# Kernel tuning notes

Measured on AMD Instinct MI355X. Metric: run time of the kernel, lower is better.

The kernel has to match this reference:

```python
import jax, jax.numpy as jnp
import numpy as np
import math

B, S, H = 8, 1024, 1024
LN_EPS = 1e-5  # assumed epsilon of create_normalization_layer('layer_norm')


def setup_inputs() -> dict:
    key = jax.random.key(0)
    ks = jax.random.split(key, 6)
    context = jax.random.normal(ks[0], (B, S, H), dtype=jnp.float32)
    mask = jnp.ones((B, 1, S), dtype=jnp.int32)
    prior = jax.random.uniform(ks[1], (B, S, S), dtype=jnp.float32)
    # LayerNorm params
    gamma = jnp.ones((H,), dtype=jnp.float32)
    beta = jnp.zeros((H,), dtype=jnp.float32)
    # Dense projections (Glorot-like init)
    scale = 1.0 / np.sqrt(H)
    Wk = jax.random.normal(ks[2], (H, H), dtype=jnp.float32) * scale
    bk = jnp.zeros((H,), dtype=jnp.float32)
    Wq = jax.random.normal(ks[3], (H, H), dtype=jnp.float32) * scale
    bq = jnp.zeros((H,), dtype=jnp.float32)
    return {"context": context, "mask": mask, "prior": prior,
            "gamma": gamma, "beta": beta, "Wk": Wk, "bk": bk, "Wq": Wq, "bq": bq}


def reference(context, mask, prior, gamma, beta, Wk, bk, Wq, bq):
    dtype = context.dtype
    s = context.shape[1]
    hs = context.shape[2]
    i = jnp.arange(s)
    adj_upper = i[:, None] == (i[None, :] - 1)          # [S,S] superdiagonal
    adj_lower = i[:, None] == (i[None, :] + 1)          # subdiagonal
    adj_mask = adj_upper | adj_lower
    pad = mask[:, 0, :].astype(bool)                    # [B,S]
    pad2d = pad[:, :, None] & pad[:, None, :]           # [B,S,S]
    final_adj = adj_mask[None, :, :] & pad2d

    # LayerNorm over last axis
    mu = jnp.mean(context, axis=-1, keepdims=True)
    var = jnp.mean(jnp.square(context - mu), axis=-1, keepdims=True)
    cn = (context - mu) * jax.lax.rsqrt(var + LN_EPS) * gamma + beta

    k = cn @ Wk + bk                                    # [B,S,H]
    q = cn @ Wq + bq
    scores = jnp.einsum('bsh,bth->bst', q, k) / math.sqrt(hs)
    scores = jnp.where(final_adj, scores, jnp.asarray(-1e9, dtype))
    neibor = jax.nn.softmax(scores, axis=-1)
    neibor = jnp.sqrt(neibor * jnp.swapaxes(neibor, 1, 2) + 1e-9)
    neibor = prior + (1.0 - prior) * neibor

    triu = i[None, :] >= i[:, None]                     # [S,S] upper incl diag
    tri = triu.astype(dtype)
    b_eye = jnp.eye(s, dtype=bool)

    t = jnp.log(neibor + 1e-9)
    t = jnp.where(adj_upper[None, :, :], t, jnp.asarray(0.0, dtype))
    t = jnp.einsum('bij,jk->bik', t, tri)               # cumulative over cols
    g = jnp.exp(jnp.einsum('ij,bjk->bik', tri, t))      # hierarchical prefix product
    keep = jnp.logical_not(jnp.logical_xor(triu, b_eye))
    g = jnp.where(keep[None, :, :], g, jnp.asarray(0.0, dtype))
    neibor_diag = jnp.where(b_eye[None, :, :], jnp.asarray(1e-9, dtype), neibor)
    g = g + jnp.swapaxes(g, 1, 2) + neibor_diag
    g = g / (jnp.sum(g, axis=-1, keepdims=True) + 1e-9)

    f2d = pad2d.astype(dtype)
    g = g * f2d
    neibor = neibor * f2d
    return g, neibor
```

## Files before the change

### kernel.cpp

```cpp
#include <hip/hip_runtime.h>
#include <hip/hip_bf16.h>

#define SB 8
#define SS 1024
#define SH 1024
#define LN_EPS 1e-5f

typedef unsigned short u16;
typedef __attribute__((ext_vector_type(8))) short bf16x8;
typedef __attribute__((ext_vector_type(4))) float f32x4;

__device__ __forceinline__ u16 f2bf(float f) {
  __hip_bfloat16 h = __float2bfloat16(f);
  return *reinterpret_cast<u16*>(&h);
}

__device__ __forceinline__ void gld16(const void* g, void* l) {
  __builtin_amdgcn_global_load_lds(
      (const __attribute__((address_space(1))) void*)g,
      (__attribute__((address_space(3))) void*)l, 16, 0, 0);
}

__global__ __launch_bounds__(256) void ln_cast(const float* __restrict__ x,
                                               const float* __restrict__ gamma,
                                               const float* __restrict__ beta,
                                               u16* __restrict__ cnb) {
  const int r = blockIdx.x;
  const int t = threadIdx.x;
  const float* xr = x + (size_t)r * SH;
  float4 v = *(const float4*)(xr + 4 * t);

  __shared__ float red[256];
  red[t] = v.x + v.y + v.z + v.w;
  __syncthreads();
#pragma unroll
  for (int off = 128; off > 0; off >>= 1) {
    if (t < off) red[t] += red[t + off];
    __syncthreads();
  }
  const float mu = red[0] * (1.0f / SH);
  __syncthreads();
  float d0 = v.x - mu, d1 = v.y - mu, d2 = v.z - mu, d3 = v.w - mu;
  red[t] = d0 * d0 + d1 * d1 + d2 * d2 + d3 * d3;
  __syncthreads();
#pragma unroll
  for (int off = 128; off > 0; off >>= 1) {
    if (t < off) red[t] += red[t + off];
    __syncthreads();
  }
  const float rstd = rsqrtf(red[0] * (1.0f / SH) + LN_EPS);

  float4 gm = *(const float4*)(gamma + 4 * t);
  float4 bt = *(const float4*)(beta + 4 * t);
  ushort4 o;
  o.x = f2bf(d0 * rstd * gm.x + bt.x);
  o.y = f2bf(d1 * rstd * gm.y + bt.y);
  o.z = f2bf(d2 * rstd * gm.z + bt.z);
  o.w = f2bf(d3 * rstd * gm.w + bt.w);
  *(ushort4*)(cnb + (size_t)r * SH + 4 * t) = o;
}

__global__ void wtrans(const float* __restrict__ Wk, const float* __restrict__ Wq,
                       u16* __restrict__ BT) {
  __shared__ float tile[32][33];
  const int n0 = blockIdx.x * 32;
  const int j0 = blockIdx.y * 32;
  const int tx = threadIdx.x, ty = threadIdx.y;
  const float* W = (n0 < 1024) ? Wq : Wk;
  const int nb = n0 & 1023;
#pragma unroll
  for (int jj = 0; jj < 4; ++jj) {
    int jl = ty + jj * 8;
    tile[jl][tx] = W[(size_t)(j0 + jl) * SH + nb + tx];
  }
  __syncthreads();
#pragma unroll
  for (int jj = 0; jj < 4; ++jj) {
    int nl = ty + jj * 8;
    BT[(size_t)(n0 + nl) * SH + j0 + tx] = f2bf(tile[tx][nl]);
  }
}

#define BM 128
#define BN 128
#define BK 32
#define GK 1024
#define GN 2048

__global__ __launch_bounds__(256) void gemm_bt(const u16* __restrict__ A,
                                               const u16* __restrict__ Bt,
                                               float* __restrict__ C) {
  __shared__ u16 As[BM * BK];
  __shared__ u16 Bs[BN * BK];
  const int tid = threadIdx.x;
  const int m0 = blockIdx.y * BM;
  const int n0 = blockIdx.x * BN;
  const int wave = tid >> 6, lane = tid & 63;
  const int wm = (wave & 1) * 64, wn = (wave >> 1) * 64;
  const int l15 = lane & 15, q = lane >> 4;

  f32x4 acc[4][4] = {};

  const int srow = tid >> 2;
  const int scol = 8 * (tid & 3);
  const u16* gA = A + (size_t)(m0 + srow) * GK + scol;
  const u16* gB = Bt + (size_t)(n0 + srow) * GK + scol;
  u16* lA = &As[srow * BK + scol];
  u16* lB = &Bs[srow * BK + scol];

  for (int k0 = 0; k0 < GK; k0 += BK) {
    __syncthreads();
    gld16(gA + k0, lA);
    gld16(gA + (size_t)64 * GK + k0, lA + 64 * BK);
    gld16(gB + k0, lB);
    gld16(gB + (size_t)64 * GK + k0, lB + 64 * BK);
    __syncthreads();

    bf16x8 af[4], bf[4];
#pragma unroll
    for (int fm = 0; fm < 4; ++fm)
      af[fm] = *(const bf16x8*)&As[(wm + fm * 16 + l15) * BK + q * 8];
#pragma unroll
    for (int fn = 0; fn < 4; ++fn)
      bf[fn] = *(const bf16x8*)&Bs[(wn + fn * 16 + l15) * BK + q * 8];
#pragma unroll
    for (int fm = 0; fm < 4; ++fm)
#pragma unroll
      for (int fn = 0; fn < 4; ++fn)
        acc[fm][fn] = __builtin_amdgcn_mfma_f32_16x16x32_bf16(
            af[fm], bf[fn], acc[fm][fn], 0, 0, 0);
  }

#pragma unroll
  for (int fm = 0; fm < 4; ++fm)
#pragma unroll
    for (int fn = 0; fn < 4; ++fn) {
      const int row0 = m0 + wm + fm * 16 + q * 4;
      const int col = n0 + wn + fn * 16 + l15;
#pragma unroll
      for (int r = 0; r < 4; ++r)
        C[(size_t)(row0 + r) * GN + col] = acc[fm][fn][r];
    }
}

__global__ __launch_bounds__(256) void adj_dots(const float* __restrict__ C,
                                                const float* __restrict__ bq,
                                                const float* __restrict__ bk,
                                                float* __restrict__ pup,
                                                float* __restrict__ pdn) {
  const int wave = threadIdx.x >> 6;
  const int lane = threadIdx.x & 63;
  const int r = blockIdx.x * 4 + wave;
  const int s = r & (SS - 1);
  const bool has_up = (s < SS - 1), has_dn = (s > 0);
  const float* qp = C + (size_t)r * GN;
  const float* kup = C + (size_t)(has_up ? r + 1 : r) * GN + SH;
  const float* kdn = C + (size_t)(has_dn ? r - 1 : r) * GN + SH;

  float du = 0.f, dd = 0.f;
#pragma unroll
  for (int v = 0; v < 4; ++v) {
    const int j = v * 256 + lane * 4;
    float4 qv = *(const float4*)(qp + j);
    float4 bqv = *(const float4*)(bq + j);
    float4 bkv = *(const float4*)(bk + j);
    const float a0 = qv.x + bqv.x, a1 = qv.y + bqv.y;
    const float a2 = qv.z + bqv.z, a3 = qv.w + bqv.w;
    if (has_up) {
      float4 ku = *(const float4*)(kup + j);
      du += a0 * (ku.x + bkv.x) + a1 * (ku.y + bkv.y) + a2 * (ku.z + bkv.z) +
            a3 * (ku.w + bkv.w);
    }
    if (has_dn) {
      float4 kd = *(const float4*)(kdn + j);
      dd += a0 * (kd.x + bkv.x) + a1 * (kd.y + bkv.y) + a2 * (kd.z + bkv.z) +
            a3 * (kd.w + bkv.w);
    }
  }
#pragma unroll
  for (int off = 32; off > 0; off >>= 1) {
    du += __shfl_down(du, off, 64);
    dd += __shfl_down(dd, off, 64);
  }
  if (lane == 0) {
    const float scale = 0.03125f;
    du *= scale;
    dd *= scale;
    float pu, pd;
    if (!has_dn) { pu = 1.f; pd = 0.f; }
    else if (!has_up) { pu = 0.f; pd = 1.f; }
    else {
      const float m = fmaxf(du, dd);
      const float eu = __expf(du - m), ed = __expf(dd - m);
      const float inv = 1.f / (eu + ed);
      pu = eu * inv;
      pd = ed * inv;
    }
    pup[r] = pu;
    pdn[r] = pd;
  }
}

__global__ __launch_bounds__(256) void rows_kernel(const float* __restrict__ prior,
                                                   const int* __restrict__ mask,
                                                   const float* __restrict__ pup,
                                                   const float* __restrict__ pdn,
                                                   float* __restrict__ g_out,
                                                   float* __restrict__ ne_out) {
  const int r = blockIdx.x;
  const int b = r >> 10, i = r & (SS - 1);
  const int t = threadIdx.x;
  const float nbz = 3.1622776601683795e-5f;
  const float nb_im1 = (i >= 1) ? sqrtf(pup[r - 1] * pdn[r] + 1e-9f) : nbz;
  const float nb_ip1 = (i <= SS - 2) ? sqrtf(pup[r] * pdn[r + 1] + 1e-9f) : nbz;

  const float* prow = prior + (size_t)r * SS;
  float4 pr = *(const float4*)(prow + 4 * t);
  const int* mrow = mask + b * SS;
  const float padi = (mrow[i] != 0) ? 1.f : 0.f;
  int4 mk = *(const int4*)(mrow + 4 * t);

  float ne[4], gsum = 0.f;
#pragma unroll
  for (int v = 0; v < 4; ++v) {
    const int k = 4 * t + v;
    const float p = (&pr.x)[v];
    const float nb = (k == i - 1) ? nb_im1 : (k == i + 1) ? nb_ip1 : nbz;
    const float n = p + (1.f - p) * nb;
    ne[v] = n;
    gsum += (k == i) ? (2.f + 1e-9f) : (1.f + n);
  }

  __shared__ float red[256];
  red[t] = gsum;
  __syncthreads();
#pragma unroll
  for (int off = 128; off > 0; off >>= 1) {
    if (t < off) red[t] += red[t + off];
    __syncthreads();
  }
  const float inv = 1.f / (red[0] + 1e-9f);

  float4 go, no;
#pragma unroll
  for (int v = 0; v < 4; ++v) {
    const int k = 4 * t + v;
    const float padk = ((&mk.x)[v] != 0) ? 1.f : 0.f;
    const float f2 = padi * padk;
    const float gt = (k == i) ? (2.f + 1e-9f) : (1.f + ne[v]);
    (&go.x)[v] = gt * inv * f2;
    (&no.x)[v] = ne[v] * f2;
  }
  *(float4*)(g_out + (size_t)r * SS + 4 * t) = go;
  *(float4*)(ne_out + (size_t)r * SS + 4 * t) = no;
}

extern "C" void kernel_launch(void* const* d_in, const int* in_sizes, int n_in,
                              void* d_out, int out_size, void* d_ws, size_t ws_size,
                              hipStream_t stream) {
  const float* context = (const float*)d_in[0];
  const int* mask = (const int*)d_in[1];
  const float* prior = (const float*)d_in[2];
  const float* gamma = (const float*)d_in[3];
  const float* beta = (const float*)d_in[4];
  const float* Wk = (const float*)d_in[5];
  const float* bk = (const float*)d_in[6];
  const float* Wq = (const float*)d_in[7];
  const float* bq = (const float*)d_in[8];

  float* out_g = (float*)d_out;
  float* out_n = out_g + (size_t)SB * SS * SS;

  char* ws = (char*)d_ws;
  u16* cnb = (u16*)ws;
  u16* BT = (u16*)(ws + ((size_t)16 << 20));
  float* Cqk = (float*)(ws + ((size_t)20 << 20));
  float* pup = (float*)(ws + ((size_t)84 << 20));
  float* pdn = (float*)(ws + ((size_t)84 << 20) + 8192 * sizeof(float));

  ln_cast<<<SB * SS, 256, 0, stream>>>(context, gamma, beta, cnb);
  wtrans<<<dim3(GN / 32, SH / 32), dim3(32, 8), 0, stream>>>(Wk, Wq, BT);
  gemm_bt<<<dim3(GN / BN, SB * SS / BM), 256, 0, stream>>>(cnb, BT, Cqk);
  adj_dots<<<SB * SS / 4, 256, 0, stream>>>(Cqk, bq, bk, pup, pdn);
  rows_kernel<<<SB * SS, 256, 0, stream>>>(prior, mask, pup, pdn, out_g, out_n);
}
```

Before: 221.2 us.

## Reassociate QK neighbor dots via precomputed Wq·Wkᵀ product and shuffle reductions

Instead of projecting the normalized context into both Q and K (an N=2048 GEMM with a large fp32 output), the code first forms the 1024x1024 product of Wk and Wq in bf16. It then computes U = cn·(Wq Wkᵀ) and takes neighbor dot products of U against the bf16 normalized rows. The bias terms that differ between the up and down neighbors are kept through a precomputed Wk·bq vector; terms that cancel in the two-way softmax are dropped. This halves the main GEMM work and its output traffic, and the transpose kernel becomes a plain cast. The LayerNorm and row-sum reductions now use wave shuffles instead of shared-memory trees. The tradeoff is an extra small GEMM, plus rounding the intermediate weight product to bf16, which may change numerical accuracy.

```diff
diff --git a/kernel.cpp b/kernel.cpp
--- a/kernel.cpp
+++ b/kernel.cpp
@@ -13,6 +13,10 @@
 __device__ __forceinline__ u16 f2bf(float f) {
   __hip_bfloat16 h = __float2bfloat16(f);
   return *reinterpret_cast<u16*>(&h);
+}
+__device__ __forceinline__ float bf2f(u16 x) {
+  unsigned v = ((unsigned)x) << 16;
+  return __builtin_bit_cast(float, v);
 }
 
 __device__ __forceinline__ void gld16(const void* g, void* l) {
@@ -27,28 +31,25 @@
                                                u16* __restrict__ cnb) {
   const int r = blockIdx.x;
   const int t = threadIdx.x;
+  const int wave = t >> 6, lane = t & 63;
   const float* xr = x + (size_t)r * SH;
   float4 v = *(const float4*)(xr + 4 * t);
 
-  __shared__ float red[256];
-  red[t] = v.x + v.y + v.z + v.w;
+  __shared__ float p1[4], p2[4];
+  float s = v.x + v.y + v.z + v.w;
+#pragma unroll
+  for (int off = 32; off > 0; off >>= 1) s += __shfl_down(s, off, 64);
+  if (lane == 0) p1[wave] = s;
   __syncthreads();
-#pragma unroll
-  for (int off = 128; off > 0; off >>= 1) {
-    if (t < off) red[t] += red[t + off];
-    __syncthreads();
-  }
-  const float mu = red[0] * (1.0f / SH);
+  const float mu = (p1[0] + p1[1] + p1[2] + p1[3]) * (1.0f / SH);
+
+  float d0 = v.x - mu, d1 = v.y - mu, d2 = v.z - mu, d3 = v.w - mu;
+  float ss = d0 * d0 + d1 * d1 + d2 * d2 + d3 * d3;
+#pragma unroll
+  for (int off = 32; off > 0; off >>= 1) ss += __shfl_down(ss, off, 64);
+  if (lane == 0) p2[wave] = ss;
   __syncthreads();
-  float d0 = v.x - mu, d1 = v.y - mu, d2 = v.z - mu, d3 = v.w - mu;
-  red[t] = d0 * d0 + d1 * d1 + d2 * d2 + d3 * d3;
-  __syncthreads();
-#pragma unroll
-  for (int off = 128; off > 0; off >>= 1) {
-    if (t < off) red[t] += red[t + off];
-    __syncthreads();
-  }
-  const float rstd = rsqrtf(red[0] * (1.0f / SH) + LN_EPS);
+  const float rstd = rsqrtf((p2[0] + p2[1] + p2[2] + p2[3]) * (1.0f / SH) + LN_EPS);
 
   float4 gm = *(const float4*)(gamma + 4 * t);
   float4 bt = *(const float4*)(beta + 4 * t);
@@ -60,36 +61,49 @@
   *(ushort4*)(cnb + (size_t)r * SH + 4 * t) = o;
 }
 
-__global__ void wtrans(const float* __restrict__ Wk, const float* __restrict__ Wq,
-                       u16* __restrict__ BT) {
-  __shared__ float tile[32][33];
-  const int n0 = blockIdx.x * 32;
-  const int j0 = blockIdx.y * 32;
-  const int tx = threadIdx.x, ty = threadIdx.y;
-  const float* W = (n0 < 1024) ? Wq : Wk;
-  const int nb = n0 & 1023;
-#pragma unroll
-  for (int jj = 0; jj < 4; ++jj) {
-    int jl = ty + jj * 8;
-    tile[jl][tx] = W[(size_t)(j0 + jl) * SH + nb + tx];
-  }
-  __syncthreads();
-#pragma unroll
-  for (int jj = 0; jj < 4; ++jj) {
-    int nl = ty + jj * 8;
-    BT[(size_t)(n0 + nl) * SH + j0 + tx] = f2bf(tile[tx][nl]);
-  }
+__global__ __launch_bounds__(256) void wcast(const float* __restrict__ Wq,
+                                             const float* __restrict__ Wk,
+                                             u16* __restrict__ Wq_bf,
+                                             u16* __restrict__ Wk_bf) {
+  const size_t e = ((size_t)blockIdx.x * 256 + threadIdx.x) * 4;
+  const size_t M = (size_t)SH * SH;
+  const float* src;
+  u16* dst;
+  if (e < M) { src = Wq + e; dst = Wq_bf + e; }
+  else       { src = Wk + (e - M); dst = Wk_bf + (e - M); }
+  float4 v = *(const float4*)src;
+  ushort4 o;
+  o.x = f2bf(v.x); o.y = f2bf(v.y); o.z = f2bf(v.z); o.w = f2bf(v.w);
+  *(ushort4*)dst = o;
+}
+
+__global__ __launch_bounds__(256) void wkbq_kernel(const float* __restrict__ Wk,
+                                                   const float* __restrict__ bq,
+                                                   float* __restrict__ wkbq) {
+  const int wave = threadIdx.x >> 6, lane = threadIdx.x & 63;
+  const int h = blockIdx.x * 4 + wave;
+  const float* row = Wk + (size_t)h * SH;
+  float s = 0.f;
+#pragma unroll
+  for (int v = 0; v < 4; ++v) {
+    const int j = v * 256 + lane * 4;
+    float4 w = *(const float4*)(row + j);
+    float4 b = *(const float4*)(bq + j);
+    s += w.x * b.x + w.y * b.y + w.z * b.z + w.w * b.w;
+  }
+#pragma unroll
+  for (int off = 32; off > 0; off >>= 1) s += __shfl_down(s, off, 64);
+  if (lane == 0) wkbq[h] = s;
 }
 
 #define BM 128
 #define BN 128
 #define BK 32
-#define GK 1024
-#define GN 2048
-
-__global__ __launch_bounds__(256) void gemm_bt(const u16* __restrict__ A,
-                                               const u16* __restrict__ Bt,
-                                               float* __restrict__ C) {
+
+template <int GKv, int GNv, bool BF16OUT>
+__global__ __launch_bounds__(256) void gemm_bt_t(const u16* __restrict__ A,
+                                                 const u16* __restrict__ Bt,
+                                                 void* __restrict__ Cv) {
   __shared__ u16 As[BM * BK];
   __shared__ u16 Bs[BN * BK];
   const int tid = threadIdx.x;
@@ -103,32 +117,32 @@
 
   const int srow = tid >> 2;
   const int scol = 8 * (tid & 3);
-  const u16* gA = A + (size_t)(m0 + srow) * GK + scol;
-  const u16* gB = Bt + (size_t)(n0 + srow) * GK + scol;
+  const u16* gA = A + (size_t)(m0 + srow) * GKv + scol;
+  const u16* gB = Bt + (size_t)(n0 + srow) * GKv + scol;
   u16* lA = &As[srow * BK + scol];
   u16* lB = &Bs[srow * BK + scol];
 
-  for (int k0 = 0; k0 < GK; k0 += BK) {
+  for (int k0 = 0; k0 < GKv; k0 += BK) {
     __syncthreads();
     gld16(gA + k0, lA);
-    gld16(gA + (size_t)64 * GK + k0, lA + 64 * BK);
+    gld16(gA + (size_t)64 * GKv + k0, lA + 64 * BK);
     gld16(gB + k0, lB);
-    gld16(gB + (size_t)64 * GK + k0, lB + 64 * BK);
+    gld16(gB + (size_t)64 * GKv + k0, lB + 64 * BK);
     __syncthreads();
 
-    bf16x8 af[4], bf[4];
+    bf16x8 af[4], bfr[4];
 #pragma unroll
     for (int fm = 0; fm < 4; ++fm)
       af[fm] = *(const bf16x8*)&As[(wm + fm * 16 + l15) * BK + q * 8];
 #pragma unroll
     for (int fn = 0; fn < 4; ++fn)
-      bf[fn] = *(const bf16x8*)&Bs[(wn + fn * 16 + l15) * BK + q * 8];
+      bfr[fn] = *(const bf16x8*)&Bs[(wn + fn * 16 + l15) * BK + q * 8];
 #pragma unroll
     for (int fm = 0; fm < 4; ++fm)
 #pragma unroll
       for (int fn = 0; fn < 4; ++fn)
         acc[fm][fn] = __builtin_amdgcn_mfma_f32_16x16x32_bf16(
-            af[fm], bf[fn], acc[fm][fn], 0, 0, 0);
+            af[fm], bfr[fn], acc[fm][fn], 0, 0, 0);
   }
 
 #pragma unroll
@@ -138,14 +152,17 @@
       const int row0 = m0 + wm + fm * 16 + q * 4;
       const int col = n0 + wn + fn * 16 + l15;
 #pragma unroll
-      for (int r = 0; r < 4; ++r)
-        C[(size_t)(row0 + r) * GN + col] = acc[fm][fn][r];
+      for (int r = 0; r < 4; ++r) {
+        const size_t idx = (size_t)(row0 + r) * GNv + col;
+        if (BF16OUT) ((u16*)Cv)[idx] = f2bf(acc[fm][fn][r]);
+        else ((float*)Cv)[idx] = acc[fm][fn][r];
+      }
     }
 }
 
-__global__ __launch_bounds__(256) void adj_dots(const float* __restrict__ C,
-                                                const float* __restrict__ bq,
-                                                const float* __restrict__ bk,
+__global__ __launch_bounds__(256) void adj_dots(const float* __restrict__ U,
+                                                const u16* __restrict__ cnb,
+                                                const float* __restrict__ wkbq,
                                                 float* __restrict__ pup,
                                                 float* __restrict__ pdn) {
   const int wave = threadIdx.x >> 6;
@@ -153,29 +170,22 @@
   const int r = blockIdx.x * 4 + wave;
   const int s = r & (SS - 1);
   const bool has_up = (s < SS - 1), has_dn = (s > 0);
-  const float* qp = C + (size_t)r * GN;
-  const float* kup = C + (size_t)(has_up ? r + 1 : r) * GN + SH;
-  const float* kdn = C + (size_t)(has_dn ? r - 1 : r) * GN + SH;
+  const float* ur = U + (size_t)r * SH;
+  const u16* up = cnb + (size_t)(has_up ? r + 1 : r) * SH;
+  const u16* dn = cnb + (size_t)(has_dn ? r - 1 : r) * SH;
 
   float du = 0.f, dd = 0.f;
 #pragma unroll
   for (int v = 0; v < 4; ++v) {
     const int j = v * 256 + lane * 4;
-    float4 qv = *(const float4*)(qp + j);
-    float4 bqv = *(const float4*)(bq + j);
-    float4 bkv = *(const float4*)(bk + j);
-    const float a0 = qv.x + bqv.x, a1 = qv.y + bqv.y;
-    const float a2 = qv.z + bqv.z, a3 = qv.w + bqv.w;
-    if (has_up) {
-      float4 ku = *(const float4*)(kup + j);
-      du += a0 * (ku.x + bkv.x) + a1 * (ku.y + bkv.y) + a2 * (ku.z + bkv.z) +
-            a3 * (ku.w + bkv.w);
-    }
-    if (has_dn) {
-      float4 kd = *(const float4*)(kdn + j);
-      dd += a0 * (kd.x + bkv.x) + a1 * (kd.y + bkv.y) + a2 * (kd.z + bkv.z) +
-            a3 * (kd.w + bkv.w);
-    }
+    float4 uv = *(const float4*)(ur + j);
+    float4 wv = *(const float4*)(wkbq + j);
+    ushort4 us = *(const ushort4*)(up + j);
+    ushort4 ds = *(const ushort4*)(dn + j);
+    const float t0 = uv.x + wv.x, t1 = uv.y + wv.y;
+    const float t2 = uv.z + wv.z, t3 = uv.w + wv.w;
+    du += bf2f(us.x) * t0 + bf2f(us.y) * t1 + bf2f(us.z) * t2 + bf2f(us.w) * t3;
+    dd += bf2f(ds.x) * t0 + bf2f(ds.y) * t1 + bf2f(ds.z) * t2 + bf2f(ds.w) * t3;
   }
 #pragma unroll
   for (int off = 32; off > 0; off >>= 1) {
@@ -210,6 +220,7 @@
   const int r = blockIdx.x;
   const int b = r >> 10, i = r & (SS - 1);
   const int t = threadIdx.x;
+  const int wave = t >> 6, lane = t & 63;
   const float nbz = 3.1622776601683795e-5f;
   const float nb_im1 = (i >= 1) ? sqrtf(pup[r - 1] * pdn[r] + 1e-9f) : nbz;
   const float nb_ip1 = (i <= SS - 2) ? sqrtf(pup[r] * pdn[r + 1] + 1e-9f) : nbz;
@@ -231,15 +242,12 @@
     gsum += (k == i) ? (2.f + 1e-9f) : (1.f + n);
   }
 
-  __shared__ float red[256];
-  red[t] = gsum;
+  __shared__ float part[4];
+#pragma unroll
+  for (int off = 32; off > 0; off >>= 1) gsum += __shfl_down(gsum, off, 64);
+  if (lane == 0) part[wave] = gsum;
   __syncthreads();
-#pragma unroll
-  for (int off = 128; off > 0; off >>= 1) {
-    if (t < off) red[t] += red[t + off];
-    __syncthreads();
-  }
-  const float inv = 1.f / (red[0] + 1e-9f);
+  const float inv = 1.f / (part[0] + part[1] + part[2] + part[3] + 1e-9f);
 
   float4 go, no;
 #pragma unroll
@@ -267,20 +275,26 @@
   const float* bk = (const float*)d_in[6];
   const float* Wq = (const float*)d_in[7];
   const float* bq = (const float*)d_in[8];
+  (void)bk;
 
   float* out_g = (float*)d_out;
   float* out_n = out_g + (size_t)SB * SS * SS;
 
   char* ws = (char*)d_ws;
   u16* cnb = (u16*)ws;
-  u16* BT = (u16*)(ws + ((size_t)16 << 20));
-  float* Cqk = (float*)(ws + ((size_t)20 << 20));
-  float* pup = (float*)(ws + ((size_t)84 << 20));
-  float* pdn = (float*)(ws + ((size_t)84 << 20) + 8192 * sizeof(float));
+  u16* Wq_bf = (u16*)(ws + ((size_t)16 << 20));
+  u16* Wk_bf = (u16*)(ws + ((size_t)18 << 20));
+  u16* PT = (u16*)(ws + ((size_t)20 << 20));
+  float* U = (float*)(ws + ((size_t)24 << 20));
+  float* wkbq = (float*)(ws + ((size_t)56 << 20));
+  float* pup = (float*)(ws + ((size_t)57 << 20));
+  float* pdn = (float*)(ws + ((size_t)57 << 20) + 8192 * sizeof(float));
 
   ln_cast<<<SB * SS, 256, 0, stream>>>(context, gamma, beta, cnb);
-  wtrans<<<dim3(GN / 32, SH / 32), dim3(32, 8), 0, stream>>>(Wk, Wq, BT);
-  gemm_bt<<<dim3(GN / BN, SB * SS / BM), 256, 0, stream>>>(cnb, BT, Cqk);
-  adj_dots<<<SB * SS / 4, 256, 0, stream>>>(Cqk, bq, bk, pup, pdn);
+  wcast<<<2048, 256, 0, stream>>>(Wq, Wk, Wq_bf, Wk_bf);
+  wkbq_kernel<<<256, 256, 0, stream>>>(Wk, bq, wkbq);
+  gemm_bt_t<1024, 1024, true><<<dim3(8, 8), 256, 0, stream>>>(Wk_bf, Wq_bf, PT);
+  gemm_bt_t<1024, 1024, false><<<dim3(8, 64), 256, 0, stream>>>(cnb, PT, U);
+  adj_dots<<<SB * SS / 4, 256, 0, stream>>>(U, cnb, wkbq, pup, pdn);
   rows_kernel<<<SB * SS, 256, 0, stream>>>(prior, mask, pup, pdn, out_g, out_n);
 }
```

Result: faster. 209.1 us (-5.5%).
